# Optimization experiments

Hardware: AMD Instinct MI355X
Metric: run time of the kernel (lower is better)

Reference implementation:

```python
import jax, jax.numpy as jnp
import numpy as np

INPUT_DIM = 20000
UNITS = 4096
NNZ = 2_000_000
BATCH = 2048


def setup_inputs() -> dict:
    key = jax.random.key(0)
    k1, k2, k3, k4 = jax.random.split(key, 4)
    x = jax.random.normal(k1, (BATCH, INPUT_DIM), dtype=jnp.float32)
    kernel_vector = jax.random.normal(k2, (NNZ,), dtype=jnp.float32) * 0.05
    bias = jnp.zeros((UNITS,), dtype=jnp.float32)
    rows = jax.random.randint(k3, (NNZ,), 0, INPUT_DIM, dtype=jnp.int32)
    cols = jax.random.randint(k4, (NNZ,), 0, UNITS, dtype=jnp.int32)
    nonzero_ind = jnp.stack([rows, cols], axis=1)  # (NNZ, 2)
    return {"x": x, "kernel_vector": kernel_vector, "bias": bias, "nonzero_ind": nonzero_ind}


def reference(x, kernel_vector, bias, nonzero_ind):
    # scatter_nd: build dense (input_dim, units) kernel from COO representation.
    # Duplicate indices accumulate (tf.scatter_nd semantics) -> use .add.
    trans = jnp.zeros((INPUT_DIM, UNITS), dtype=kernel_vector.dtype)
    trans = trans.at[nonzero_ind[:, 0], nonzero_ind[:, 1]].add(kernel_vector)
    out = x @ trans + bias  # (batch, units)
    return jnp.tanh(out)
```

## Files before the change

kernel.cpp:

```cpp
#include <hip/hip_runtime.h>
#include <cstdint>
#include <cstddef>

#define M_DIM 2048
#define N_DIM 4096
#define K_DIM 20000
#define KP    20480
#define KZ    10240
#define GSTEPS 160
#define WBT_BYTES  167772160UL
#define XB_OFFSET  167772160UL
#define CP_OFFSET  251658240UL

typedef __attribute__((ext_vector_type(8))) short short8;
typedef __attribute__((ext_vector_type(4))) float float4v;
typedef __attribute__((ext_vector_type(8))) unsigned short ushort8;

__device__ __forceinline__ unsigned short f2bf_rne(float f) {
    union { float f; unsigned int u; } v; v.f = f;
    unsigned int u = v.u;
    u += 0x7FFFu + ((u >> 16) & 1u);
    return (unsigned short)(u >> 16);
}

__device__ __forceinline__ float bf2f(unsigned short h) {
    union { unsigned int u; float f; } v;
    v.u = ((unsigned int)h) << 16;
    return v.f;
}

__device__ __forceinline__ void gload_lds16(const void* g, void* l) {
    __builtin_amdgcn_global_load_lds(
        (const __attribute__((address_space(1))) void*)g,
        (__attribute__((address_space(3))) void*)l, 16, 0, 0);
}

__global__ void scatter_bf16_kernel(const float* __restrict__ kv,
                                    const int* __restrict__ ind,
                                    unsigned int* __restrict__ W, int nnz) {
    int t = blockIdx.x * blockDim.x + threadIdx.x;
    if (t >= nnz) return;
    int r = ind[2 * t];
    int c = ind[2 * t + 1];
    float v = kv[t];
    size_t elem = (size_t)c * KP + r;
    unsigned int* word = &W[elem >> 1];
    const bool hi = (elem & 1) != 0;
    unsigned int old = __atomic_load_n(word, __ATOMIC_RELAXED);
    unsigned int assumed;
    do {
        assumed = old;
        unsigned short h = hi ? (unsigned short)(assumed >> 16)
                              : (unsigned short)(assumed & 0xFFFFu);
        unsigned short nh = f2bf_rne(bf2f(h) + v);
        unsigned int nw = hi ? ((assumed & 0x0000FFFFu) | ((unsigned int)nh << 16))
                             : ((assumed & 0xFFFF0000u) | (unsigned int)nh);
        old = atomicCAS(word, assumed, nw);
    } while (old != assumed);
}

__global__ void convert_kernel(const float* __restrict__ src,
                               unsigned short* __restrict__ dst) {
    size_t t = (size_t)blockIdx.x * 256 + threadIdx.x;
    int row = (int)(t / 2560);
    int c8  = (int)(t % 2560);
    ushort8 o;
    if (c8 < 2500) {
        const float4* sv = (const float4*)(src + (size_t)row * K_DIM + (size_t)c8 * 8);
        float4 a = sv[0];
        float4 b = sv[1];
        o[0] = f2bf_rne(a.x); o[1] = f2bf_rne(a.y);
        o[2] = f2bf_rne(a.z); o[3] = f2bf_rne(a.w);
        o[4] = f2bf_rne(b.x); o[5] = f2bf_rne(b.y);
        o[6] = f2bf_rne(b.z); o[7] = f2bf_rne(b.w);
    } else {
        o = (ushort8)0;
    }
    *(ushort8*)(dst + (size_t)row * KP + (size_t)c8 * 8) = o;
}

__global__ __launch_bounds__(512, 2) void gemm256_kernel(
    const unsigned short* __restrict__ A,
    const unsigned short* __restrict__ Bt,
    float* __restrict__ Cp) {

    __shared__ unsigned short L[65536];

    const int t    = threadIdx.x;
    const int w    = t >> 6;
    const int l    = t & 63;
    const int quad = l >> 4;
    const int r16  = l & 15;
    const int wm   = w >> 2;
    const int wn   = w & 3;

    const int m0 = blockIdx.y * 256;
    const int n0 = blockIdx.x * 256;
    const size_t k0 = (size_t)blockIdx.z * KZ;

    const int sl  = (l & 7) ^ (l >> 3);
    const int rst = w * 8 + (l >> 3);
    const unsigned short* gA[4];
    const unsigned short* gB[4];
#pragma unroll
    for (int j = 0; j < 4; ++j) {
        gA[j] = A  + (size_t)(m0 + j * 64 + rst) * KP + k0 + sl * 8;
        gB[j] = Bt + (size_t)(n0 + j * 64 + rst) * KP + k0 + sl * 8;
    }
    char* Lb = (char*)L;

    auto STAGE = [&](int cb) {
#pragma unroll
        for (int j = 0; j < 4; ++j) {
            gload_lds16(gA[j], Lb + cb + j * 8192 + (w << 10));
            gload_lds16(gB[j], Lb + cb + 32768 + j * 8192 + (w << 10));
            gA[j] += 64; gB[j] += 64;
        }
    };

    const int h   = r16 & 7;
    const int so0 = ((quad ^ h) << 4);
    const int so1 = (((4 | quad) ^ h) << 4);
    const int arow = wm * 16384 + r16 * 128;
    const int brow = wn * 8192  + r16 * 128;

    float4v acc[8][4];
#pragma unroll
    for (int i = 0; i < 8; ++i)
#pragma unroll
        for (int j = 0; j < 4; ++j)
            acc[i][j] = (float4v){0.f, 0.f, 0.f, 0.f};

    STAGE(0);
    STAGE(65536);
    asm volatile("s_waitcnt vmcnt(8)" ::: "memory");
    __builtin_amdgcn_s_barrier();

    for (int ks = 0; ks < GSTEPS; ++ks) {
        const int cb = (ks & 1) << 16;
        const char* Ab = Lb + cb;
        const char* Bb = Lb + cb + 32768;

        short8 bf0[4], bf1[4], afA[4], afB[4];

#pragma unroll
        for (int j = 0; j < 4; ++j) bf0[j] = *(const short8*)(Bb + brow + j * 2048 + so0);
#pragma unroll
        for (int i = 0; i < 4; ++i) afA[i] = *(const short8*)(Ab + arow + i * 2048 + so0);
        __builtin_amdgcn_s_setprio(1);
#pragma unroll
        for (int i = 0; i < 4; ++i)
#pragma unroll
            for (int j = 0; j < 4; ++j)
                acc[i][j] = __builtin_amdgcn_mfma_f32_16x16x32_bf16(afA[i], bf0[j], acc[i][j], 0, 0, 0);
        __builtin_amdgcn_s_setprio(0);

#pragma unroll
        for (int j = 0; j < 4; ++j) bf1[j] = *(const short8*)(Bb + brow + j * 2048 + so1);
#pragma unroll
        for (int i = 0; i < 4; ++i) afB[i] = *(const short8*)(Ab + arow + i * 2048 + so1);
        __builtin_amdgcn_s_setprio(1);
#pragma unroll
        for (int i = 0; i < 4; ++i)
#pragma unroll
            for (int j = 0; j < 4; ++j)
                acc[i][j] = __builtin_amdgcn_mfma_f32_16x16x32_bf16(afB[i], bf1[j], acc[i][j], 0, 0, 0);
        __builtin_amdgcn_s_setprio(0);

#pragma unroll
        for (int i = 0; i < 4; ++i) afA[i] = *(const short8*)(Ab + arow + (i + 4) * 2048 + so0);
        __builtin_amdgcn_s_setprio(1);
#pragma unroll
        for (int i = 0; i < 4; ++i)
#pragma unroll
            for (int j = 0; j < 4; ++j)
                acc[i + 4][j] = __builtin_amdgcn_mfma_f32_16x16x32_bf16(afA[i], bf0[j], acc[i + 4][j], 0, 0, 0);
        __builtin_amdgcn_s_setprio(0);

#pragma unroll
        for (int i = 0; i < 4; ++i) afB[i] = *(const short8*)(Ab + arow + (i + 4) * 2048 + so1);
        __builtin_amdgcn_s_setprio(1);
#pragma unroll
        for (int i = 0; i < 4; ++i)
#pragma unroll
            for (int j = 0; j < 4; ++j)
                acc[i + 4][j] = __builtin_amdgcn_mfma_f32_16x16x32_bf16(afB[i], bf1[j], acc[i + 4][j], 0, 0, 0);
        __builtin_amdgcn_s_setprio(0);

        asm volatile("s_waitcnt lgkmcnt(0)" ::: "memory");
        __builtin_amdgcn_s_barrier();
        if (ks < GSTEPS - 2) {
            STAGE(cb);
            asm volatile("s_waitcnt vmcnt(8)" ::: "memory");
        } else if (ks == GSTEPS - 2) {
            asm volatile("s_waitcnt vmcnt(0)" ::: "memory");
        }
        __builtin_amdgcn_s_barrier();
    }

    float* Cz = Cp + (size_t)blockIdx.z * ((size_t)M_DIM * N_DIM);
#pragma unroll
    for (int i = 0; i < 8; ++i) {
        const int row = m0 + wm * 128 + i * 16 + quad * 4;
#pragma unroll
        for (int j = 0; j < 4; ++j) {
            const int col = n0 + wn * 64 + j * 16 + r16;
#pragma unroll
            for (int r = 0; r < 4; ++r)
                Cz[(size_t)(row + r) * N_DIM + col] = acc[i][j][r];
        }
    }
}

__global__ void combine_kernel(const float* __restrict__ Cp,
                               const float* __restrict__ bias,
                               float* __restrict__ out) {
    size_t t = (size_t)blockIdx.x * 256 + threadIdx.x;
    const size_t stride = (size_t)M_DIM * N_DIM / 4;
    float4 a = ((const float4*)Cp)[t];
    float4 b = ((const float4*)Cp)[t + stride];
    float4 bv = ((const float4*)bias)[t & (N_DIM / 4 - 1)];
    float4 o;
    o.x = tanhf(a.x + b.x + bv.x);
    o.y = tanhf(a.y + b.y + bv.y);
    o.z = tanhf(a.z + b.z + bv.z);
    o.w = tanhf(a.w + b.w + bv.w);
    ((float4*)out)[t] = o;
}

extern "C" void kernel_launch(void* const* d_in, const int* in_sizes, int n_in,
                              void* d_out, int out_size, void* d_ws, size_t ws_size,
                              hipStream_t stream) {
    const float* x    = (const float*)d_in[0];
    const float* kv   = (const float*)d_in[1];
    const float* bias = (const float*)d_in[2];
    const int*   ind  = (const int*)d_in[3];
    const int nnz = in_sizes[1];

    unsigned short* Wbt = (unsigned short*)d_ws;
    unsigned short* xb  = (unsigned short*)((char*)d_ws + XB_OFFSET);
    float* Cp = (float*)((char*)d_ws + CP_OFFSET);

    hipMemsetAsync(Wbt, 0, WBT_BYTES, stream);
    scatter_bf16_kernel<<<(nnz + 255) / 256, 256, 0, stream>>>(
        kv, ind, (unsigned int*)Wbt, nnz);
    convert_kernel<<<(M_DIM * (KP / 8)) / 256, 256, 0, stream>>>(x, xb);
    gemm256_kernel<<<dim3(N_DIM / 256, M_DIM / 256, 2), 512, 0, stream>>>(
        xb, Wbt, Cp);
    combine_kernel<<<(M_DIM * N_DIM) / (256 * 4), 256, 0, stream>>>(
        Cp, bias, (float*)d_out);
}
```

Baseline: 715.2 us.

## Restructure GEMM mainloop into 4-slot K32 pipeline with staggered A/B staging

Changes the GEMM main loop from double-buffered K64 stages to a four-slot ring of K32 half-tiles. Global-to-LDS loads for A and B are issued separately, interleaved between MFMA phases. The XOR swizzle on the LDS layout is dropped in favour of a plain 64-byte row stride. The goal is finer-grained overlap of loads with MFMA work and a deeper prefetch distance, at the cost of more barriers per K step and possible LDS bank conflicts from the unswizzled layout.

```diff
diff --git a/kernel.cpp b/kernel.cpp
--- a/kernel.cpp
+++ b/kernel.cpp
@@ -7,7 +7,7 @@
 #define K_DIM 20000
 #define KP    20480
 #define KZ    10240
-#define GSTEPS 160
+#define NITER 80
 #define WBT_BYTES  167772160UL
 #define XB_OFFSET  167772160UL
 #define CP_OFFSET  251658240UL
@@ -98,31 +98,27 @@
     const int n0 = blockIdx.x * 256;
     const size_t k0 = (size_t)blockIdx.z * KZ;
 
-    const int sl  = (l & 7) ^ (l >> 3);
-    const int rst = w * 8 + (l >> 3);
-    const unsigned short* gA[4];
-    const unsigned short* gB[4];
-#pragma unroll
-    for (int j = 0; j < 4; ++j) {
-        gA[j] = A  + (size_t)(m0 + j * 64 + rst) * KP + k0 + sl * 8;
-        gB[j] = Bt + (size_t)(n0 + j * 64 + rst) * KP + k0 + sl * 8;
-    }
+    const int l4 = l >> 2;
+    const int c4 = l & 3;
+    const unsigned short* pA0 = A  + (size_t)(m0 + w * 32 + l4) * KP + k0 + c4 * 8;
+    const unsigned short* pA1 = pA0 + (size_t)16 * KP;
+    const unsigned short* pB0 = Bt + (size_t)(n0 + w * 32 + l4) * KP + k0 + c4 * 8;
+    const unsigned short* pB1 = pB0 + (size_t)16 * KP;
+
     char* Lb = (char*)L;
-
-    auto STAGE = [&](int cb) {
-#pragma unroll
-        for (int j = 0; j < 4; ++j) {
-            gload_lds16(gA[j], Lb + cb + j * 8192 + (w << 10));
-            gload_lds16(gB[j], Lb + cb + 32768 + j * 8192 + (w << 10));
-            gA[j] += 64; gB[j] += 64;
-        }
-    };
-
-    const int h   = r16 & 7;
-    const int so0 = ((quad ^ h) << 4);
-    const int so1 = (((4 | quad) ^ h) << 4);
-    const int arow = wm * 16384 + r16 * 128;
-    const int brow = wn * 8192  + r16 * 128;
+    const int wdst = w << 11;
+
+#define STAGE_A(REG) do { \
+    gload_lds16(pA0, Lb + (REG) + wdst); \
+    gload_lds16(pA1, Lb + (REG) + wdst + 1024); \
+    pA0 += 32; pA1 += 32; } while (0)
+#define STAGE_B(REG) do { \
+    gload_lds16(pB0, Lb + (REG) + wdst); \
+    gload_lds16(pB1, Lb + (REG) + wdst + 1024); \
+    pB0 += 32; pB1 += 32; } while (0)
+
+    const int aoff = (wm * 128 + r16) * 64 + quad * 16;
+    const int boff = 32768 + (wn * 64 + r16) * 64 + quad * 16;
 
     float4v acc[8][4];
 #pragma unroll
@@ -131,72 +127,54 @@
         for (int j = 0; j < 4; ++j)
             acc[i][j] = (float4v){0.f, 0.f, 0.f, 0.f};
 
-    STAGE(0);
-    STAGE(65536);
+    short8 bfr[4], af[4];
+
+#define VM8 asm volatile("s_waitcnt vmcnt(8)" ::: "memory")
+#define VMNONE ((void)0)
+
+#define PHASE(BASEOFF, MH, LOADB, STG, VM) do { \
+    const char* base_ = Lb + (BASEOFF); \
+    if (LOADB) { \
+        _Pragma("unroll") \
+        for (int j = 0; j < 4; ++j) \
+            bfr[j] = *(const short8*)(base_ + boff + j * 1024); \
+    } \
+    _Pragma("unroll") \
+    for (int i = 0; i < 4; ++i) \
+        af[i] = *(const short8*)(base_ + aoff + (MH) * 4096 + i * 1024); \
+    STG; \
+    __builtin_amdgcn_s_barrier(); \
+    asm volatile("s_waitcnt lgkmcnt(0)" ::: "memory"); \
+    __builtin_amdgcn_s_setprio(1); \
+    _Pragma("unroll") \
+    for (int i = 0; i < 4; ++i) \
+        _Pragma("unroll") \
+        for (int j = 0; j < 4; ++j) \
+            acc[(MH) * 4 + i][j] = __builtin_amdgcn_mfma_f32_16x16x32_bf16( \
+                af[i], bfr[j], acc[(MH) * 4 + i][j], 0, 0, 0); \
+    __builtin_amdgcn_s_setprio(0); \
+    VM; \
+    __builtin_amdgcn_s_barrier(); \
+} while (0)
+
+    STAGE_A(0);     STAGE_B(32768);
+    STAGE_A(16384); STAGE_B(49152);
+    STAGE_A(65536); STAGE_B(98304);
     asm volatile("s_waitcnt vmcnt(8)" ::: "memory");
     __builtin_amdgcn_s_barrier();
 
-    for (int ks = 0; ks < GSTEPS; ++ks) {
-        const int cb = (ks & 1) << 16;
-        const char* Ab = Lb + cb;
-        const char* Bb = Lb + cb + 32768;
-
-        short8 bf0[4], bf1[4], afA[4], afB[4];
-
-#pragma unroll
-        for (int j = 0; j < 4; ++j) bf0[j] = *(const short8*)(Bb + brow + j * 2048 + so0);
-#pragma unroll
-        for (int i = 0; i < 4; ++i) afA[i] = *(const short8*)(Ab + arow + i * 2048 + so0);
-        __builtin_amdgcn_s_setprio(1);
-#pragma unroll
-        for (int i = 0; i < 4; ++i)
-#pragma unroll
-            for (int j = 0; j < 4; ++j)
-                acc[i][j] = __builtin_amdgcn_mfma_f32_16x16x32_bf16(afA[i], bf0[j], acc[i][j], 0, 0, 0);
-        __builtin_amdgcn_s_setprio(0);
-
-#pragma unroll
-        for (int j = 0; j < 4; ++j) bf1[j] = *(const short8*)(Bb + brow + j * 2048 + so1);
-#pragma unroll
-        for (int i = 0; i < 4; ++i) afB[i] = *(const short8*)(Ab + arow + i * 2048 + so1);
-        __builtin_amdgcn_s_setprio(1);
-#pragma unroll
-        for (int i = 0; i < 4; ++i)
-#pragma unroll
-            for (int j = 0; j < 4; ++j)
-                acc[i][j] = __builtin_amdgcn_mfma_f32_16x16x32_bf16(afB[i], bf1[j], acc[i][j], 0, 0, 0);
-        __builtin_amdgcn_s_setprio(0);
-
-#pragma unroll
-        for (int i = 0; i < 4; ++i) afA[i] = *(const short8*)(Ab + arow + (i + 4) * 2048 + so0);
-        __builtin_amdgcn_s_setprio(1);
-#pragma unroll
-        for (int i = 0; i < 4; ++i)
-#pragma unroll
-            for (int j = 0; j < 4; ++j)
-                acc[i + 4][j] = __builtin_amdgcn_mfma_f32_16x16x32_bf16(afA[i], bf0[j], acc[i + 4][j], 0, 0, 0);
-        __builtin_amdgcn_s_setprio(0);
-
-#pragma unroll
-        for (int i = 0; i < 4; ++i) afB[i] = *(const short8*)(Ab + arow + (i + 4) * 2048 + so1);
-        __builtin_amdgcn_s_setprio(1);
-#pragma unroll
-        for (int i = 0; i < 4; ++i)
-#pragma unroll
-            for (int j = 0; j < 4; ++j)
-                acc[i + 4][j] = __builtin_amdgcn_mfma_f32_16x16x32_bf16(afB[i], bf1[j], acc[i + 4][j], 0, 0, 0);
-        __builtin_amdgcn_s_setprio(0);
-
-        asm volatile("s_waitcnt lgkmcnt(0)" ::: "memory");
-        __builtin_amdgcn_s_barrier();
-        if (ks < GSTEPS - 2) {
-            STAGE(cb);
-            asm volatile("s_waitcnt vmcnt(8)" ::: "memory");
-        } else if (ks == GSTEPS - 2) {
-            asm volatile("s_waitcnt vmcnt(0)" ::: "memory");
-        }
-        __builtin_amdgcn_s_barrier();
+#pragma unroll 1
+    for (int it = 0; it < NITER; ++it) {
+        PHASE(0,     0, true,  STAGE_A(81920),  VMNONE);
+        PHASE(0,     1, false, STAGE_B(114688), VM8);
+        PHASE(16384, 0, true,  STAGE_A(0),      VMNONE);
+        PHASE(16384, 1, false, STAGE_B(32768),  VM8);
+        PHASE(65536, 0, true,  STAGE_A(16384),  VMNONE);
+        PHASE(65536, 1, false, STAGE_B(49152),  VM8);
+        PHASE(81920, 0, true,  STAGE_A(65536),  VMNONE);
+        PHASE(81920, 1, false, STAGE_B(98304),  VM8);
     }
+    asm volatile("s_waitcnt vmcnt(0)" ::: "memory");
 
     float* Cz = Cp + (size_t)blockIdx.z * ((size_t)M_DIM * N_DIM);
 #pragma unroll
@@ -210,6 +188,11 @@
                 Cz[(size_t)(row + r) * N_DIM + col] = acc[i][j][r];
         }
     }
+#undef PHASE
+#undef STAGE_A
+#undef STAGE_B
+#undef VM8
+#undef VMNONE
 }
 
 __global__ void combine_kernel(const float* __restrict__ Cp,
```

After: 662.9 us. 7.3% less time.
